# Optimization experiments

Measured on AMD Instinct MI355X. Metric: run time of the kernel, lower is better.

## Reference

```python
import jax, jax.numpy as jnp
import numpy as np

H = 512        # rnn_h
E = 256        # embedding_dim
ATD = 32       # action_type_emb_dim
VOCAB = 50000  # data_agent.wordcnt
NUM_ACTIONS = 10
CHECK_WEIGHT = 1.0
B, SIN, SOUT, Y = 32, 128, 32, 256
DIN = 2 * H + 1 + E + ATD + E  # dec_gru input size (y_in=True, bidir=True)


def gru_step(h, x, Wih, Whh, bih, bhh):
    # PyTorch GRUCell math
    gi = x @ Wih.T + bih
    gh = h @ Whh.T + bhh
    ir, iz, i_n = jnp.split(gi, 3, axis=-1)
    hr, hz, h_n = jnp.split(gh, 3, axis=-1)
    r = jax.nn.sigmoid(ir + hr)
    z = jax.nn.sigmoid(iz + hz)
    n = jnp.tanh(i_n + r * h_n)
    return (1.0 - z) * n + z * h


def setup_inputs() -> dict:
    key = jax.random.key(0)
    ks = iter(jax.random.split(key, 48))

    def p(shape, scale=0.05):
        return jax.random.normal(next(ks), shape, dtype=jnp.float32) * scale

    inp = {}
    inp["x"] = jax.random.randint(next(ks), (B, SIN), 0, VOCAB)
    inp["action_key"] = jax.random.randint(next(ks), (Y,), 0, VOCAB)
    inp["action_type"] = jax.random.randint(next(ks), (Y,), 0, NUM_ACTIONS + 1)
    inp["current_room"] = jax.random.randint(next(ks), (B, SOUT), 0, VOCAB)
    inp["checked"] = jax.random.uniform(next(ks), (B, SOUT + 1, Y), dtype=jnp.float32)
    inp["y"] = jax.random.uniform(next(ks), (B, SOUT, Y), dtype=jnp.float32)
    emb = p((VOCAB, E))
    inp["emb_table"] = emb.at[0].set(0.0)  # padding_idx=0
    inp["atype_table"] = p((NUM_ACTIONS + 1, ATD))
    # encoder GRU, bidirectional, 1 layer
    inp["enc_Wih_f"] = p((3 * H, E)); inp["enc_Whh_f"] = p((3 * H, H))
    inp["enc_bih_f"] = p((3 * H,));   inp["enc_bhh_f"] = p((3 * H,))
    inp["enc_Wih_b"] = p((3 * H, E)); inp["enc_Whh_b"] = p((3 * H, H))
    inp["enc_bih_b"] = p((3 * H,));   inp["enc_bhh_b"] = p((3 * H,))
    inp["trans_W"] = p((E, 2 * H)); inp["trans_b"] = p((E,))
    inp["merge_W"] = p((H, 2 * H)); inp["merge_b"] = p((H,))
    inp["dec_Wih"] = p((3 * H, DIN)); inp["dec_Whh"] = p((3 * H, H))
    inp["dec_bih"] = p((3 * H,));     inp["dec_bhh"] = p((3 * H,))
    inp["dec_W"] = p((1, H)); inp["dec_b"] = p((1,))
    inp["chk_W1"] = p((H, 2 * H + ATD + H)); inp["chk_b1"] = p((H,))
    inp["chk_W2"] = p((1, H));               inp["chk_b2"] = p((1,))
    return inp


def reference(x, action_key, action_type, current_room, checked, y,
              emb_table, atype_table,
              enc_Wih_f, enc_Whh_f, enc_bih_f, enc_bhh_f,
              enc_Wih_b, enc_Whh_b, enc_bih_b, enc_bhh_b,
              trans_W, trans_b, merge_W, merge_b,
              dec_Wih, dec_Whh, dec_bih, dec_bhh, dec_W, dec_b,
              chk_W1, chk_b1, chk_W2, chk_b2):
    emb_out = emb_table[x]  # [B, SIN, E]

    def enc_scan(Wih, Whh, bih, bhh, xs):  # xs: [S, B, E]
        def step(h, xt):
            h2 = gru_step(h, xt, Wih, Whh, bih, bhh)
            return h2, h2
        h0 = jnp.zeros((B, H), emb_out.dtype)
        return jax.lax.scan(step, h0, xs)

    xs = emb_out.transpose(1, 0, 2)
    hT_f, hs_f = enc_scan(enc_Wih_f, enc_Whh_f, enc_bih_f, enc_bhh_f, xs)
    hT_b, hs_b = enc_scan(enc_Wih_b, enc_Whh_b, enc_bih_b, enc_bhh_b, xs[::-1])
    hs_b = hs_b[::-1]
    enc_out = jnp.concatenate([hs_f, hs_b], axis=-1).transpose(1, 0, 2)  # [B, SIN, 2H]

    action_emb = emb_table[action_key]  # [Y, E]
    trans_out = jnp.tanh(enc_out @ trans_W.T + trans_b)  # [B, SIN, E]
    scores = (jnp.einsum('bse,ye->bys', emb_out, action_emb)
              + jnp.einsum('bse,ye->bys', trans_out, action_emb))
    alpha = jax.nn.softmax(scores, axis=-1)
    attention = jnp.einsum('bys,bsd->byd', alpha, enc_out)  # [B, Y, 2H]

    atype_exp = jnp.broadcast_to(atype_table[action_type], (B, Y, ATD))
    room_emb = emb_table[current_room]  # [B, SOUT, E]

    # faithful to torch: hidden [2,B,H].view(B, 2H) (layer-major flatten)
    hidden_cat = jnp.stack([hT_f, hT_b], 0).reshape(B, 2 * H)
    h0_dec = jnp.tanh(hidden_cat @ merge_W.T + merge_b)  # [B, H]
    h_dec = jnp.broadcast_to(h0_dec[:, None, :], (B, Y, H)).reshape(B * Y, H)

    y_prev = jnp.concatenate([jnp.zeros((B, 1, Y), y.dtype), y[:, :-1]], axis=1)

    att_flat = attention.reshape(B * Y, 2 * H)
    at_flat = atype_exp.reshape(B * Y, ATD)

    xs_scan = (checked[:, :SOUT].transpose(1, 0, 2),   # check_in  [T,B,Y]
               room_emb.transpose(1, 0, 2),            # room      [T,B,E]
               y_prev.transpose(1, 0, 2),              # y_{t-1}   [T,B,Y]
               y.transpose(1, 0, 2),                   # y_t       [T,B,Y]
               checked[:, 1:].transpose(1, 0, 2))      # check tgt [T,B,Y]

    def step(h, inputs):
        chk_t, room_t, yp_t, y_t, chk_next = inputs
        room_in = jnp.broadcast_to(room_t[:, None, :], (B, Y, E))
        y_in = jnp.broadcast_to((yp_t @ action_emb)[:, None, :], (B, Y, E))
        dec_in = jnp.concatenate(
            [attention, chk_t[..., None], room_in, atype_exp, y_in], axis=-1
        ).reshape(B * Y, DIN)
        h2 = gru_step(h, dec_in, dec_Wih, dec_Whh, dec_bih, dec_bhh)
        logits = (h2 @ dec_W.T + dec_b).reshape(B, Y)
        logp = jax.nn.log_softmax(logits, axis=1)
        l = -(logp * y_t).sum()
        cat = jnp.concatenate([att_flat, at_flat, h2], axis=1)
        chk = jax.nn.sigmoid(jnp.tanh(cat @ chk_W1.T + chk_b1) @ chk_W2.T + chk_b2).reshape(B, Y)
        cl = -((chk_next * jnp.log(chk) + (1.0 - chk_next) * jnp.log(1.0 - chk)) * y_t).sum() * CHECK_WEIGHT
        return h2, (l, cl)

    _, (ls, cls) = jax.lax.scan(step, h_dec, xs_scan)
    ysum = y.sum()
    loss = ls.sum() / ysum
    check_loss = cls.sum() / ysum
    return (loss + check_loss, loss, check_loss)
```

## Files before the change

kernel.cpp:

```cpp
#include <hip/hip_runtime.h>

typedef unsigned short ushort;
typedef unsigned int uint;
typedef __attribute__((ext_vector_type(8))) short short8;
typedef __attribute__((ext_vector_type(4))) float f32x4;
typedef __attribute__((ext_vector_type(4))) uint u32x4;

#define DEVI __device__ __forceinline__

#define B_ 32
#define SIN_ 128
#define SOUT_ 32
#define Y_ 256
#define H_ 512
#define E_ 256
#define TH_ 1536

DEVI float b2f(ushort u){ return __uint_as_float(((uint)u)<<16); }
DEVI ushort f2b(float f){ uint x = __float_as_uint(f); return (ushort)((x + 0x7FFFu + ((x>>16)&1u)) >> 16); }
DEVI float sigf(float x){ return 1.f/(1.f+__expf(-x)); }
DEVI float tanh_fast(float x){ return 2.f/(1.f+__expf(-2.f*x)) - 1.f; }
DEVI float splus(float x){ return fmaxf(x,0.f) + log1pf(__expf(-fabsf(x))); }
DEVI short8 cvt8(u32x4 v){ return __builtin_bit_cast(short8, v); }

DEVI uint ld_flag(const uint* p){
  uint r;
  asm volatile("global_load_dword %0, %1, off sc0 sc1\n\ts_waitcnt vmcnt(0)"
               : "=v"(r) : "v"(p) : "memory");
  return r;
}
DEVI void st_flag(uint* p, uint v){
  asm volatile("global_store_dword %0, %1, off sc0 sc1" :: "v"(p), "v"(v) : "memory");
}
DEVI void st_h16(ushort* p, uint v){
  asm volatile("global_store_short %0, %1, off sc0 sc1" :: "v"(p), "v"(v) : "memory");
}

__global__ void k_init(float* acc){ if (threadIdx.x < 4) acc[threadIdx.x] = 0.f; }

__global__ void k_wsfail(float* out){ out[0]=1.2345e8f; out[1]=2.3456e8f; out[2]=3.4567e8f; }

__global__ void k_init_enc(uint* __restrict__ flags, ushort* __restrict__ hG)
{
  const int id = blockIdx.x*256 + threadIdx.x;
  if (id < 256) flags[id] = 0u;
  if (id < 16384) ((uint4*)hG)[id] = make_uint4(0,0,0,0);
}

__global__ __launch_bounds__(256) void k_ysum(const float* __restrict__ yv, float* __restrict__ acc)
{
  __shared__ float red[256];
  float s = 0.f;
  for (long i = (long)blockIdx.x*256 + threadIdx.x; i < (long)B_*SOUT_*Y_; i += (long)gridDim.x*256) s += yv[i];
  red[threadIdx.x] = s; __syncthreads();
  for (int o=128;o;o>>=1){ if ((int)threadIdx.x<o) red[threadIdx.x] += red[threadIdx.x+o]; __syncthreads(); }
  if (threadIdx.x==0) atomicAdd(acc+2, red[0]);
}

__global__ void k_lookup(const int* __restrict__ x, const int* __restrict__ akey,
                         const int* __restrict__ atype, const int* __restrict__ croom,
                         const float* __restrict__ yv,
                         const float* __restrict__ emb, const float* __restrict__ attab,
                         ushort* __restrict__ embxs, ushort* __restrict__ aemb,
                         ushort* __restrict__ aembT, float* __restrict__ avec,
                         ushort* __restrict__ acat, ushort* __restrict__ yprev)
{
  const long N1 = (long)SIN_*B_*E_;
  const long N2 = (long)Y_*E_;
  const long N3 = (long)Y_*32;
  const long N4 = (long)SOUT_*B_*E_;
  const long N5 = (long)SOUT_*B_*Y_;
  for (long i = (long)blockIdx.x*blockDim.x + threadIdx.x; i < N1+N2+N3+N4+N5; i += (long)gridDim.x*blockDim.x){
    long id = i;
    if (id < N1){
      int e = id & 255; long sb = id >> 8; int bb = (int)(sb & 31); int s = (int)(sb >> 5);
      embxs[id] = f2b(emb[(size_t)x[bb*SIN_ + s]*E_ + e]);
    } else if ((id -= N1) < N2){
      int e = (int)(id & 255), yy = (int)(id >> 8);
      ushort v = f2b(emb[(size_t)akey[yy]*E_ + e]);
      aemb[yy*E_ + e] = v;
      aembT[e*Y_ + yy] = v;
    } else if ((id -= N2) < N3){
      int a = (int)(id & 31), yy = (int)(id >> 5);
      avec[yy*32 + a] = attab[atype[yy]*32 + a];
    } else if ((id -= N3) < N4){
      int e = (int)(id & 255); long tb = id >> 8; int bb = (int)(tb & 31); int t = (int)(tb >> 5);
      acat[(size_t)tb*512 + e] = f2b(emb[(size_t)croom[bb*SOUT_ + t]*E_ + e]);
    } else { id -= N4;
      int yy = (int)(id & 255); long tb = id >> 8; int bb = (int)(tb & 31); int t = (int)(tb >> 5);
      yprev[id] = (t == 0) ? (ushort)0 : f2b(yv[((size_t)bb*SOUT_ + (t-1))*Y_ + yy]);
    }
  }
}

__global__ __launch_bounds__(256)
void k_convall(const float* __restrict__ eWihF, const float* __restrict__ eWihB,
               const float* __restrict__ transW, const float* __restrict__ dWih,
               const float* __restrict__ cW1, const float* __restrict__ dWhh,
               ushort* __restrict__ WihFb, ushort* __restrict__ WihBb,
               ushort* __restrict__ Wtrb, ushort* __restrict__ Wattb,
               ushort* __restrict__ Wcat2b, ushort* __restrict__ W1attb,
               ushort* __restrict__ Wdecb, ushort* __restrict__ Wchk2b)
{
  const long N1 = 393216;
  const long N2 = 393216;
  const long N3 = 262144;
  const long N4 = 1572864;
  const long N5 = 393216;
  const long N6 = 393216;
  const long N7 = 524288;
  const long N8 = 786432;
  const long N9 = 262144;
  const long NT = N1+N2+N3+N4+N5+N6+N7+N8+N9;
  for (long i = (long)blockIdx.x*256 + threadIdx.x; i < NT; i += (long)gridDim.x*256){
    long id = i;
    if (id < N1){ WihFb[id] = f2b(eWihF[id]); }
    else if ((id -= N1) < N2){ WihBb[id] = f2b(eWihB[id]); }
    else if ((id -= N2) < N3){ Wtrb[id] = f2b(transW[id]); }
    else if ((id -= N3) < N4){
      const long r = id>>10, c = id&1023;
      Wattb[id] = f2b(dWih[r*1569 + c]);
    }
    else if ((id -= N4) < N5){
      const long r = id>>8, c = id&255;
      Wcat2b[r*512 + c] = f2b(dWih[r*1569 + 1025 + c]);
    }
    else if ((id -= N5) < N6){
      const long r = id>>8, c = id&255;
      Wcat2b[r*512 + 256 + c] = f2b(dWih[r*1569 + 1313 + c]);
    }
    else if ((id -= N6) < N7){
      const long r = id>>10, c = id&1023;
      W1attb[id] = f2b(cW1[r*1568 + c]);
    }
    else if ((id -= N7) < N8){ Wdecb[id] = f2b(dWhh[id]); }
    else { id -= N8;
      const long r = id>>9, c = id&511;
      Wchk2b[id] = f2b(cW1[r*1568 + 1056 + c]);
    }
  }
}

__global__ void k_prep2(const float* __restrict__ avec, const float* __restrict__ decWih,
                        const float* __restrict__ dbih, const float* __restrict__ cW1,
                        const float* __restrict__ cb1, const float* __restrict__ dbhh,
                        float* __restrict__ addy, float* __restrict__ addcy,
                        float* __restrict__ wchk, float* __restrict__ dbhhrz)
{
  const long NA = (long)Y_*TH_;
  const long NB = (long)Y_*H_;
  for (long i = (long)blockIdx.x*blockDim.x + threadIdx.x; i < NA+NB+TH_+TH_; i += (long)gridDim.x*blockDim.x){
    long id = i;
    if (id < NA){
      int n = (int)(id % TH_), yy = (int)(id / TH_);
      float s = dbih[n];
      const float* wr = decWih + (size_t)n*1569 + 1281;
      const float* av = avec + yy*32;
      #pragma unroll
      for (int a=0;a<32;++a) s += av[a]*wr[a];
      addy[id] = s;
    } else if ((id -= NA) < NB){
      int n = (int)(id & 511), yy = (int)(id >> 9);
      float s = cb1[n];
      const float* wr = cW1 + (size_t)n*1568 + 1024;
      const float* av = avec + yy*32;
      #pragma unroll
      for (int a=0;a<32;++a) s += av[a]*wr[a];
      addcy[id] = s;
    } else if ((id -= NB) < TH_){
      wchk[id] = decWih[(size_t)id*1569 + 1024];
    } else { id -= TH_;
      dbhhrz[id] = (id < 1024) ? dbhh[id] : 0.f;
    }
  }
}

#define GF_BIAS 1
#define GF_TANH 2
#define GF_WF32 4
#define GF_WBF16 8
#define GF_ADDY 32
#define GF_CHK 64
#define GF_ESUM 128

template<int FLAGS>
__global__ __launch_bounds__(256)
void gemm_nt(const ushort* __restrict__ A, const ushort* __restrict__ W,
             const float* __restrict__ bias,
             const float* __restrict__ addy, int lday,
             float* __restrict__ Cf, ushort* __restrict__ Cb, int ldC,
             int K, int ldA, int ldW, int n0,
             long zA, long zW, long zC,
             const ushort* __restrict__ chkbase)
{
  const int z = blockIdx.z;
  A += (long)z*zA; W += (long)z*zW;
  const int bn = n0 + (blockIdx.x<<7);
  const int bm = (blockIdx.y<<7);
  const int tid = threadIdx.x;
  const int w = tid>>6, lane = tid&63;
  const int wm = (w>>1)<<6, wn = (w&1)<<6;
  const int rs = tid>>1;
  const int kh = (tid&1)<<5;
  __shared__ ushort lsA[8192];
  __shared__ ushort lsB[8192];
  f32x4 acc[4][4];
  #pragma unroll
  for (int i=0;i<4;++i)
    #pragma unroll
    for (int jj=0;jj<4;++jj) acc[i][jj] = 0.f;

  const ushort* pa = A + (size_t)(bm+rs)*ldA + kh;
  const ushort* pb = W + (size_t)(bn+rs)*ldW + kh;
  uint4 va[4], vb[4];
  #pragma unroll
  for (int i=0;i<4;++i){ va[i] = *(const uint4*)(pa + i*8); vb[i] = *(const uint4*)(pb + i*8); }
  const int nkt = K>>6;
  for (int kt=0; kt<nkt; ++kt){
    __syncthreads();
    #pragma unroll
    for (int i=0;i<4;++i){
      const int c = ((tid&1)<<2) + i;
      *(uint4*)&lsA[(size_t)((c<<7) + rs)<<3] = va[i];
      *(uint4*)&lsB[(size_t)((c<<7) + rs)<<3] = vb[i];
    }
    __syncthreads();
    if (kt+1 < nkt){
      const ushort* qa = pa + (size_t)(kt+1)*64;
      const ushort* qb = pb + (size_t)(kt+1)*64;
      #pragma unroll
      for (int i=0;i<4;++i){ va[i] = *(const uint4*)(qa + i*8); vb[i] = *(const uint4*)(qb + i*8); }
    }
    #pragma unroll
    for (int ks=0;ks<2;++ks){
      const int ch = (ks<<2) + (lane>>4);
      short8 af[4], bf[4];
      #pragma unroll
      for (int mi=0;mi<4;++mi) af[mi] = *(const short8*)&lsA[(size_t)((ch<<7) + wm + (mi<<4) + (lane&15))<<3];
      #pragma unroll
      for (int ni=0;ni<4;++ni) bf[ni] = *(const short8*)&lsB[(size_t)((ch<<7) + wn + (ni<<4) + (lane&15))<<3];
      #pragma unroll
      for (int mi=0;mi<4;++mi)
        #pragma unroll
        for (int ni=0;ni<4;++ni)
          acc[mi][ni] = __builtin_amdgcn_mfma_f32_16x16x32_bf16(af[mi], bf[ni], acc[mi][ni], 0,0,0);
    }
  }
  if (FLAGS & GF_CHK){
    float rsum[4][4];
    #pragma unroll
    for (int mi=0;mi<4;++mi)
      #pragma unroll
      for (int q=0;q<4;++q) rsum[mi][q] = 0.f;
    #pragma unroll
    for (int mi=0;mi<4;++mi){
      #pragma unroll
      for (int ni=0;ni<4;++ni){
        const int col = bn + wn + (ni<<4) + (lane&15);
        const float w2v = addy[col];
        const int row0 = bm + wm + (mi<<4) + ((lane>>4)<<2);
        #pragma unroll
        for (int q=0;q<4;++q){
          const float u = acc[mi][ni][q] + b2f(chkbase[(size_t)(row0+q)*H_ + col]);
          rsum[mi][q] += tanh_fast(u) * w2v;
        }
      }
    }
    #pragma unroll
    for (int mi=0;mi<4;++mi)
      #pragma unroll
      for (int q=0;q<4;++q){
        float v = rsum[mi][q];
        v += __shfl_xor(v,1); v += __shfl_xor(v,2); v += __shfl_xor(v,4); v += __shfl_xor(v,8);
        if ((lane&15)==0){
          const int row = bm + wm + (mi<<4) + ((lane>>4)<<2) + q;
          atomicAdd(&Cf[row], v);
        }
      }
  } else {
    const long zc = (long)z*zC;
    #pragma unroll
    for (int mi=0;mi<4;++mi){
      #pragma unroll
      for (int ni=0;ni<4;++ni){
        const int col = bn + wn + (ni<<4) + (lane&15);
        const int row0 = bm + wm + (mi<<4) + ((lane>>4)<<2);
        float bv = 0.f;
        if (FLAGS & GF_BIAS) bv = bias[col];
        #pragma unroll
        for (int q=0;q<4;++q){
          const int row = row0 + q;
          float xv = acc[mi][ni][q] + bv;
          if (FLAGS & GF_ADDY) xv += addy[(size_t)(row&255)*lday + col];
          if (FLAGS & GF_TANH) xv = tanh_fast(xv);
          if (FLAGS & GF_ESUM) xv += b2f(chkbase[((size_t)(row&127)*32 + (row>>7))*256 + col]);
          if (FLAGS & GF_WF32)  Cf[zc + (size_t)row*ldC + col] = xv;
          if (FLAGS & GF_WBF16) Cb[zc + (size_t)row*ldC + col] = f2b(xv);
        }
      }
    }
  }
}

__global__ __launch_bounds__(256,1)
void enc_persist(const float* __restrict__ Wf, const float* __restrict__ Wb,
                 const float* __restrict__ bhf, const float* __restrict__ bhb,
                 const ushort* __restrict__ gif, const ushort* __restrict__ gib,
                 ushort* __restrict__ hG, uint* __restrict__ flags,
                 ushort* __restrict__ encout, ushort* __restrict__ encoutT,
                 float* __restrict__ hTf, float* __restrict__ hTb)
{
  const int g = blockIdx.x;
  const int dir = g >> 5;
  const int j0 = (g & 31) << 4;
  const int tid = threadIdx.x;
  const int w = tid >> 6, lane = tid & 63;
  const int mi = w & 1, kh = w >> 1;
  const int l15 = lane & 15, l4 = lane >> 4;
  const int brow0 = mi*16 + l4*4;

  const float* W = dir ? Wb : Wf;
  const float* bh = dir ? bhb : bhf;
  const ushort* gi = dir ? gib : gif;

  __shared__ __align__(16) float cred[2][3][256];
  __shared__ float bhl[48];

  short8 bw[3][8];
  {
    const int kbase = kh*256 + l4*8;
    #pragma unroll
    for (int ni=0; ni<3; ++ni){
      const float* wr = W + (size_t)(ni*512 + j0 + l15)*512 + kbase;
      #pragma unroll
      for (int ks=0; ks<8; ++ks){
        const float4 f0 = *(const float4*)(wr + ks*32);
        const float4 f1 = *(const float4*)(wr + ks*32 + 4);
        short8 v;
        v[0]=(short)f2b(f0.x); v[1]=(short)f2b(f0.y); v[2]=(short)f2b(f0.z); v[3]=(short)f2b(f0.w);
        v[4]=(short)f2b(f1.x); v[5]=(short)f2b(f1.y); v[6]=(short)f2b(f1.z); v[7]=(short)f2b(f1.w);
        bw[ni][ks] = v;
      }
    }
  }
  if (tid < 48) bhl[tid] = bh[(tid>>4)*512 + j0 + (tid&15)];
  __syncthreads();

  float bh0r=0.f, bh1r=0.f, bh2r=0.f;
  if (kh==0){ bh0r = bhl[l15]; bh1r = bhl[16+l15]; bh2r = bhl[32+l15]; }
  float holdr[4] = {0.f,0.f,0.f,0.f};
  uint* myflag = flags + dir*32 + (g&31);

  for (int t=0; t<128; ++t){
    const int tt = dir ? (127 - t) : t;
    float giv0[4], giv1[4], giv2[4];
    if (kh==0){
      const ushort* girow = gi + ((size_t)tt*32 + brow0)*1536 + j0 + l15;
      #pragma unroll
      for (int q=0; q<4; ++q){
        giv0[q] = b2f(girow[q*1536]);
        giv1[q] = b2f(girow[q*1536 + 512]);
        giv2[q] = b2f(girow[q*1536 + 1024]);
      }
    }
    if (t){
      if ((tid>>6)==2 && (tid&63)<32){
        const uint* fp = flags + dir*32 + (tid&31);
        while (ld_flag(fp) < (uint)t) __builtin_amdgcn_s_sleep(2);
      }
      __syncthreads();
    }
    const ushort* hsrc = hG + ((size_t)((t&1)*2 + dir))*32768 + (size_t)(mi*16+l15)*1024 + kh*256 + l4*8;
    u32x4 a0,a1,a2,a3,a4,a5,a6,a7,b0,b1,b2,b3,b4,b5,b6,b7;
    asm volatile(
      "global_load_dwordx4 %0, %16, off sc0 sc1\n\t"
      "global_load_dwordx4 %1, %16, off offset:64 sc0 sc1\n\t"
      "global_load_dwordx4 %2, %16, off offset:128 sc0 sc1\n\t"
      "global_load_dwordx4 %3, %16, off offset:192 sc0 sc1\n\t"
      "global_load_dwordx4 %4, %16, off offset:256 sc0 sc1\n\t"
      "global_load_dwordx4 %5, %16, off offset:320 sc0 sc1\n\t"
      "global_load_dwordx4 %6, %16, off offset:384 sc0 sc1\n\t"
      "global_load_dwordx4 %7, %16, off offset:448 sc0 sc1\n\t"
      "global_load_dwordx4 %8, %16, off offset:1024 sc0 sc1\n\t"
      "global_load_dwordx4 %9, %16, off offset:1088 sc0 sc1\n\t"
      "global_load_dwordx4 %10, %16, off offset:1152 sc0 sc1\n\t"
      "global_load_dwordx4 %11, %16, off offset:1216 sc0 sc1\n\t"
      "global_load_dwordx4 %12, %16, off offset:1280 sc0 sc1\n\t"
      "global_load_dwordx4 %13, %16, off offset:1344 sc0 sc1\n\t"
      "global_load_dwordx4 %14, %16, off offset:1408 sc0 sc1\n\t"
      "global_load_dwordx4 %15, %16, off offset:1472 sc0 sc1\n\t"
      "s_waitcnt vmcnt(0)"
      : "=&v"(a0),"=&v"(a1),"=&v"(a2),"=&v"(a3),"=&v"(a4),"=&v"(a5),"=&v"(a6),"=&v"(a7),
        "=&v"(b0),"=&v"(b1),"=&v"(b2),"=&v"(b3),"=&v"(b4),"=&v"(b5),"=&v"(b6),"=&v"(b7)
      : "v"(hsrc)
      : "memory");
    const short8 ah[8] = {cvt8(a0),cvt8(a1),cvt8(a2),cvt8(a3),cvt8(a4),cvt8(a5),cvt8(a6),cvt8(a7)};
    const short8 al[8] = {cvt8(b0),cvt8(b1),cvt8(b2),cvt8(b3),cvt8(b4),cvt8(b5),cvt8(b6),cvt8(b7)};
    f32x4 acc[3]; acc[0]=0.f; acc[1]=0.f; acc[2]=0.f;
    #pragma unroll
    for (int ks=0; ks<8; ++ks){
      acc[0] = __builtin_amdgcn_mfma_f32_16x16x32_bf16(ah[ks], bw[0][ks], acc[0],0,0,0);
      acc[1] = __builtin_amdgcn_mfma_f32_16x16x32_bf16(ah[ks], bw[1][ks], acc[1],0,0,0);
      acc[2] = __builtin_amdgcn_mfma_f32_16x16x32_bf16(ah[ks], bw[2][ks], acc[2],0,0,0);
      acc[0] = __builtin_amdgcn_mfma_f32_16x16x32_bf16(al[ks], bw[0][ks], acc[0],0,0,0);
      acc[1] = __builtin_amdgcn_mfma_f32_16x16x32_bf16(al[ks], bw[1][ks], acc[1],0,0,0);
      acc[2] = __builtin_amdgcn_mfma_f32_16x16x32_bf16(al[ks], bw[2][ks], acc[2],0,0,0);
    }
    if (kh==1){
      #pragma unroll
      for (int ni=0; ni<3; ++ni) *(f32x4*)&cred[mi][ni][lane*4] = acc[ni];
    }
    __syncthreads();
    if (kh==0){
      #pragma unroll
      for (int ni=0; ni<3; ++ni){
        const f32x4 o = *(const f32x4*)&cred[mi][ni][lane*4];
        acc[ni][0]+=o[0]; acc[ni][1]+=o[1]; acc[ni][2]+=o[2]; acc[ni][3]+=o[3];
      }
      ushort* dst = hG + ((size_t)(((t+1)&1)*2 + dir))*32768;
      #pragma unroll
      for (int q=0; q<4; ++q){
        const int b = brow0 + q;
        const float r  = sigf(giv0[q] + acc[0][q] + bh0r);
        const float zg = sigf(giv1[q] + acc[1][q] + bh1r);
        const float n  = tanh_fast(giv2[q] + r*(acc[2][q] + bh2r));
        const float h2 = (1.f - zg)*n + zg*holdr[q];
        holdr[q] = h2;
        const ushort hb = f2b(h2);
        const ushort hl = f2b(h2 - b2f(hb));
        if (t < 127){
          st_h16(dst + (size_t)b*1024 + j0 + l15, (uint)hb);
          st_h16(dst + (size_t)b*1024 + 512 + j0 + l15, (uint)hl);
        }
        encout[((size_t)b*SIN_ + tt)*1024 + dir*H_ + j0 + l15] = hb;
        encoutT[((size_t)b*1024 + dir*H_ + j0 + l15)*SIN_ + tt] = hb;
      }
    }
    __syncthreads();
    if (t < 127 && tid == 0) st_flag(myflag, (uint)(t+1));
  }
  if (kh==0){
    float* hT = dir ? hTb : hTf;
    #pragma unroll
    for (int q=0; q<4; ++q) hT[(size_t)(brow0+q)*H_ + j0 + l15] = holdr[q];
  }
}

__global__ __launch_bounds__(256) void k_softmax(const float* __restrict__ sc, ushort* __restrict__ al)
{
  const int row = blockIdx.x*4 + (threadIdx.x>>6);
  const int lane = threadIdx.x&63;
  const float* s = sc + (size_t)row*SIN_;
  const float2 v = *(const float2*)&s[lane*2];
  float m = fmaxf(v.x, v.y);
  #pragma unroll
  for (int o=1;o<64;o<<=1) m = fmaxf(m, __shfl_xor(m, o));
  const float e0 = __expf(v.x - m), e1 = __expf(v.y - m);
  float sum = e0 + e1;
  #pragma unroll
  for (int o=1;o<64;o<<=1) sum += __shfl_xor(sum, o);
  const float inv = 1.f/sum;
  ushort* a = al + (size_t)row*SIN_;
  const uint pkv = (uint)f2b(e0*inv) | ((uint)f2b(e1*inv)<<16);
  *(uint*)&a[lane*2] = pkv;
}

__global__ __launch_bounds__(512)
void k_merge(const float* __restrict__ hTf, const float* __restrict__ hTb,
             const float* __restrict__ mW, const float* __restrict__ mb,
             float* __restrict__ h0)
{
  const int b = blockIdx.x, j = threadIdx.x;
  __shared__ float hc[1024];
  for (int i=j; i<1024; i+=512){
    const int half = i >> 9, jj = i & 511;
    hc[i] = (b < 16) ? hTf[(size_t)(2*b + half)*H_ + jj] : hTb[(size_t)(2*(b-16) + half)*H_ + jj];
  }
  __syncthreads();
  float d = mb[j];
  const float* wr = mW + (size_t)j*1024;
  #pragma unroll 8
  for (int k=0;k<1024;k+=4){
    const float4 a = *(const float4*)&wr[k];
    const float4 hh = *(const float4*)&hc[k];
    d += a.x*hh.x + a.y*hh.y + a.z*hh.z + a.w*hh.w;
  }
  h0[(size_t)b*H_ + j] = tanh_fast(d);
}

__global__ void k_bcast(const float* __restrict__ h0, ushort* __restrict__ hb,
                        float* __restrict__ chkdot, float* __restrict__ logits)
{
  for (long i = (long)blockIdx.x*blockDim.x + threadIdx.x; i < (long)8192*H_; i += (long)gridDim.x*blockDim.x){
    const int jj = (int)(i & 511); const long row = i >> 9; const int bb = (int)(row >> 8);
    hb[i] = f2b(h0[(size_t)bb*H_ + jj]);
    if (i < 8192){ chkdot[i] = 0.f; logits[i] = 0.f; }
  }
}

__global__ __launch_bounds__(512,1)
void gemm_dec(const ushort* __restrict__ A, const ushort* __restrict__ Wd,
              const ushort* __restrict__ gib, const float* __restrict__ sproj_t,
              const float* __restrict__ wchk, const float* __restrict__ dbhh,
              const float* __restrict__ checked, int t,
              const float* __restrict__ decW,
              ushort* __restrict__ h2bo, float* __restrict__ logits)
{
  const int bx = blockIdx.x;
  const int by = blockIdx.y;
  const int bm = by<<7;
  const int tid = threadIdx.x;
  const int w = tid>>6, lane = tid&63;
  const int wrh = w>>2, wc = w&3;
  const int wm = wrh<<6;
  const int l15 = lane&15, l4 = lane>>4;
  __shared__ ushort lsA[128*72];
  __shared__ ushort lsB[384*72];
  f32x4 acc[3][4][2];
  #pragma unroll
  for (int gg=0;gg<3;++gg)
    #pragma unroll
    for (int mi2=0;mi2<4;++mi2)
      #pragma unroll
      for (int ni2=0;ni2<2;++ni2) acc[gg][mi2][ni2] = 0.f;

  const int saRow0 = tid>>3, saK = (tid&7)<<3;
  uint4 va[2], vb[6];
  {
    #pragma unroll
    for (int i=0;i<2;++i){
      const int row = saRow0 + (i<<6);
      va[i] = *(const uint4*)&A[(size_t)(bm+row)*512 + saK];
    }
    #pragma unroll
    for (int i=0;i<6;++i){
      const int s = tid + (i<<9);
      const int gg = s>>10, w1 = s&1023, row = w1>>3, kc = (w1&7)<<3;
      vb[i] = *(const uint4*)&Wd[(size_t)((gg<<9) + (bx<<7) + row)*512 + kc];
    }
  }
  for (int kt=0; kt<8; ++kt){
    __syncthreads();
    #pragma unroll
    for (int i=0;i<2;++i){
      const int row = saRow0 + (i<<6);
      *(uint4*)&lsA[row*72 + saK] = va[i];
    }
    #pragma unroll
    for (int i=0;i<6;++i){
      const int s = tid + (i<<9);
      const int gg = s>>10, w1 = s&1023, row = w1>>3, kc = (w1&7)<<3;
      *(uint4*)&lsB[((gg<<7)+row)*72 + kc] = vb[i];
    }
    __syncthreads();
    if (kt < 7){
      const int ko = (kt+1)<<6;
      #pragma unroll
      for (int i=0;i<2;++i){
        const int row = saRow0 + (i<<6);
        va[i] = *(const uint4*)&A[(size_t)(bm+row)*512 + ko + saK];
      }
      #pragma unroll
      for (int i=0;i<6;++i){
        const int s = tid + (i<<9);
        const int gg = s>>10, w1 = s&1023, row = w1>>3, kc = (w1&7)<<3;
        vb[i] = *(const uint4*)&Wd[(size_t)((gg<<9) + (bx<<7) + row)*512 + ko + kc];
      }
    }
    #pragma unroll
    for (int ks=0;ks<2;++ks){
      short8 af[4];
      #pragma unroll
      for (int mi2=0;mi2<4;++mi2)
        af[mi2] = *(const short8*)&lsA[(wm + (mi2<<4) + l15)*72 + (ks<<5) + (l4<<3)];
      short8 bf[3][2];
      #pragma unroll
      for (int gg=0;gg<3;++gg)
        #pragma unroll
        for (int ni2=0;ni2<2;++ni2)
          bf[gg][ni2] = *(const short8*)&lsB[((gg<<7) + (wc<<5) + (ni2<<4) + l15)*72 + (ks<<5) + (l4<<3)];
      #pragma unroll
      for (int gg=0;gg<3;++gg)
        #pragma unroll
        for (int mi2=0;mi2<4;++mi2)
          #pragma unroll
          for (int ni2=0;ni2<2;++ni2)
            acc[gg][mi2][ni2] = __builtin_amdgcn_mfma_f32_16x16x32_bf16(af[mi2], bf[gg][ni2], acc[gg][mi2][ni2], 0,0,0);
    }
  }
  const int bb = by>>1;
  const float* sp = sproj_t + (size_t)bb*TH_;
  const int jbase = (bx<<7) + (wc<<5);
  float spv[3][2], wcv[3][2], bhnv[2], dwv[2];
  #pragma unroll
  for (int ni2=0;ni2<2;++ni2){
    const int j = jbase + (ni2<<4) + l15;
    spv[0][ni2] = sp[j]; spv[1][ni2] = sp[512+j]; spv[2][ni2] = sp[1024+j];
    wcv[0][ni2] = wchk[j]; wcv[1][ni2] = wchk[512+j]; wcv[2][ni2] = wchk[1024+j];
    bhnv[ni2] = dbhh[1024+j];
    dwv[ni2] = decW[j];
  }
  const float* ckrow = checked + ((size_t)(bb*33 + t))*Y_;
  float lrow[4][4];
  #pragma unroll
  for (int mi2=0;mi2<4;++mi2)
    #pragma unroll
    for (int q=0;q<4;++q) lrow[mi2][q] = 0.f;
  #pragma unroll
  for (int mi2=0;mi2<4;++mi2){
    #pragma unroll
    for (int q=0;q<4;++q){
      const int row = bm + wm + (mi2<<4) + (l4<<2) + q;
      const float ck = ckrow[row & 255];
      #pragma unroll
      for (int ni2=0;ni2<2;++ni2){
        const int j = jbase + (ni2<<4) + l15;
        const float g0 = b2f(gib[(size_t)row*TH_ + j]);
        const float g1 = b2f(gib[(size_t)row*TH_ + 512 + j]);
        const float g2 = b2f(gib[(size_t)row*TH_ + 1024 + j]);
        const float hold = b2f(A[(size_t)row*H_ + j]);
        const float r  = sigf(g0 + spv[0][ni2] + ck*wcv[0][ni2] + acc[0][mi2][ni2][q]);
        const float zg = sigf(g1 + spv[1][ni2] + ck*wcv[1][ni2] + acc[1][mi2][ni2][q]);
        const float n  = tanh_fast(g2 + spv[2][ni2] + ck*wcv[2][ni2] + r*(acc[2][mi2][ni2][q] + bhnv[ni2]));
        const float h2 = (1.f - zg)*n + zg*hold;
        h2bo[(size_t)row*H_ + j] = f2b(h2);
        lrow[mi2][q] += h2 * dwv[ni2];
      }
    }
  }
  #pragma unroll
  for (int mi2=0;mi2<4;++mi2)
    #pragma unroll
    for (int q=0;q<4;++q){
      float v = lrow[mi2][q];
      v += __shfl_xor(v,1); v += __shfl_xor(v,2); v += __shfl_xor(v,4); v += __shfl_xor(v,8);
      if (l15==0){
        const int row = bm + wm + (mi2<<4) + (l4<<2) + q;
        atomicAdd(&logits[row], v);
      }
    }
}

__global__ __launch_bounds__(256)
void dec_loss(float* __restrict__ chkdot, const float* __restrict__ cb2v,
              const float* __restrict__ checked, const float* __restrict__ yv,
              float* __restrict__ logits, int t, float* __restrict__ acc)
{
  const int tid = threadIdx.x;
  if (blockIdx.x < 32){
    const int row = blockIdx.x*256 + tid;
    const int bb = row>>8, yy = row&255;
    const float u = chkdot[row] + cb2v[0];
    chkdot[row] = 0.f;
    const float c = checked[((size_t)bb*33 + (t+1))*Y_ + yy];
    const float yt = yv[((size_t)bb*SOUT_ + t)*Y_ + yy];
    float wv = yt * (c*splus(-u) + (1.f-c)*splus(u));
    __shared__ float red[256];
    red[tid] = wv; __syncthreads();
    for (int o=128;o;o>>=1){ if (tid<o) red[tid] += red[tid+o]; __syncthreads(); }
    if (tid==0) atomicAdd(acc+1, red[0]);
  } else {
    __shared__ float red[256];
    __shared__ float bmx[32], bsm[32];
    const int bb = tid>>3, part = tid&7;
    float lv[32];
    const float* lg = logits + bb*Y_ + part*32;
    float m = -1e30f;
    #pragma unroll
    for (int i=0;i<32;++i){ lv[i] = lg[i]; m = fmaxf(m, lv[i]); }
    red[tid] = m; __syncthreads();
    if (part==0){ float mm = red[tid];
      #pragma unroll
      for (int k2=1;k2<8;++k2) mm = fmaxf(mm, red[tid+k2]);
      bmx[bb] = mm; }
    __syncthreads();
    const float bm = bmx[bb];
    float se = 0.f;
    #pragma unroll
    for (int i=0;i<32;++i) se += __expf(lv[i]-bm);
    red[tid] = se; __syncthreads();
    if (part==0){ float ss = 0.f;
      #pragma unroll
      for (int k2=0;k2<8;++k2) ss += red[tid+k2];
      bsm[bb] = ss; }
    __syncthreads();
    const float lse = bm + logf(bsm[bb]);
    const float* yr = yv + ((size_t)bb*SOUT_ + t)*Y_ + part*32;
    float pl = 0.f;
    #pragma unroll
    for (int i=0;i<32;++i) pl += yr[i]*(lv[i]-lse);
    red[tid] = pl; __syncthreads();
    if (tid==0){ float s = 0.f;
      for (int k2=0;k2<256;++k2) s += red[k2];
      atomicAdd(acc+0, -s); }
    __syncthreads();
    for (int i=tid; i<8192; i+=256) logits[i] = 0.f;
  }
}

__global__ void k_final(const float* __restrict__ acc, float* __restrict__ out)
{
  if (threadIdx.x==0){
    const float ls = acc[0], cls = acc[1], ys = acc[2];
    out[0] = (ls+cls)/ys; out[1] = ls/ys; out[2] = cls/ys;
  }
}

extern "C" void kernel_launch(void* const* d_in, const int* in_sizes, int n_in,
                              void* d_out, int out_size, void* d_ws, size_t ws_size,
                              hipStream_t stream)
{
  (void)in_sizes; (void)n_in; (void)out_size;
  const int*   x      = (const int*)d_in[0];
  const int*   akey   = (const int*)d_in[1];
  const int*   atype  = (const int*)d_in[2];
  const int*   croom  = (const int*)d_in[3];
  const float* checked= (const float*)d_in[4];
  const float* yv     = (const float*)d_in[5];
  const float* emb    = (const float*)d_in[6];
  const float* attab  = (const float*)d_in[7];
  const float* eWihF  = (const float*)d_in[8];
  const float* eWhhF  = (const float*)d_in[9];
  const float* ebihF  = (const float*)d_in[10];
  const float* ebhhF  = (const float*)d_in[11];
  const float* eWihB  = (const float*)d_in[12];
  const float* eWhhB  = (const float*)d_in[13];
  const float* ebihB  = (const float*)d_in[14];
  const float* ebhhB  = (const float*)d_in[15];
  const float* transW = (const float*)d_in[16];
  const float* transb = (const float*)d_in[17];
  const float* mergeW = (const float*)d_in[18];
  const float* mergeb = (const float*)d_in[19];
  const float* dWih   = (const float*)d_in[20];
  const float* dWhh   = (const float*)d_in[21];
  const float* dbih   = (const float*)d_in[22];
  const float* dbhh   = (const float*)d_in[23];
  const float* dW     = (const float*)d_in[24];
  const float* cW1    = (const float*)d_in[26];
  const float* cb1    = (const float*)d_in[27];
  const float* cW2    = (const float*)d_in[28];
  const float* cb2    = (const float*)d_in[29];

  char* base = (char*)d_ws;
  size_t off = 0;
  auto alloc = [&](size_t bytes)->char*{ char* p = base + off; off += (bytes + 255) & ~(size_t)255; return p; };

  float*  accv   = (float*)alloc(256);
  ushort* embxs  = (ushort*)alloc((size_t)SIN_*B_*E_*2);
  ushort* aemb   = (ushort*)alloc((size_t)Y_*E_*2);
  ushort* aembT  = (ushort*)alloc((size_t)Y_*E_*2);
  float*  avec   = (float*)alloc((size_t)Y_*32*4);
  ushort* yprev  = (ushort*)alloc((size_t)SOUT_*B_*Y_*2);
  ushort* acat   = (ushort*)alloc((size_t)SOUT_*B_*512*2);
  ushort* gi_fb  = (ushort*)alloc((size_t)2*SIN_*B_*TH_*2);
  ushort* gi_f   = gi_fb;
  ushort* gi_b   = gi_fb + (size_t)SIN_*B_*TH_;
  ushort* gibase = gi_fb;
  ushort* encout = (ushort*)alloc((size_t)B_*SIN_*1024*2);
  ushort* encoutT= (ushort*)alloc((size_t)B_*1024*SIN_*2);
  float*  hTf    = (float*)alloc((size_t)B_*H_*4);
  float*  hTb    = (float*)alloc((size_t)B_*H_*4);
  float*  h0dec  = (float*)alloc((size_t)B_*H_*4);
  ushort* esum   = (ushort*)alloc((size_t)B_*SIN_*E_*2);
  float*  scores = (float*)alloc((size_t)B_*Y_*SIN_*4);
  ushort* alpha  = (ushort*)alloc((size_t)B_*Y_*SIN_*2);
  ushort* att    = (ushort*)alloc((size_t)8192*1024*2);
  ushort* chkbase= (ushort*)alloc((size_t)8192*H_*2);
  float*  addy   = (float*)alloc((size_t)Y_*TH_*4);
  float*  addcy  = (float*)alloc((size_t)Y_*H_*4);
  float*  sproj  = (float*)alloc((size_t)SOUT_*B_*TH_*4);
  float*  wchk   = (float*)alloc((size_t)TH_*4);
  float*  dbhhrz = (float*)alloc((size_t)TH_*4);
  ushort* WihFb  = (ushort*)alloc((size_t)TH_*E_*2);
  ushort* WihBb  = (ushort*)alloc((size_t)TH_*E_*2);
  ushort* Wtrb   = (ushort*)alloc((size_t)E_*1024*2);
  ushort* Wattb  = (ushort*)alloc((size_t)TH_*1024*2);
  ushort* Wcat2b = (ushort*)alloc((size_t)TH_*512*2);
  ushort* W1attb = (ushort*)alloc((size_t)H_*1024*2);
  ushort* Wdecb  = (ushort*)alloc((size_t)TH_*512*2);
  ushort* Wchk2b = (ushort*)alloc((size_t)512*512*2);
  ushort* h2bA   = (ushort*)alloc((size_t)8192*H_*2);
  ushort* h2bB   = (ushort*)alloc((size_t)8192*H_*2);
  float*  chkdot = (float*)alloc((size_t)8192*4);
  float*  logits = (float*)alloc((size_t)8192*4);
  ushort* hG     = (ushort*)alloc((size_t)2*2*32*1024*2);
  uint*   flags  = (uint*)alloc((size_t)256*4);

  if (off > ws_size){ k_wsfail<<<1,1,0,stream>>>((float*)d_out); return; }

  float* outp = (float*)d_out;

  k_init<<<dim3(1), dim3(64), 0, stream>>>(accv);
  k_init_enc<<<dim3(64), dim3(256), 0, stream>>>(flags, hG);
  k_ysum<<<dim3(256), dim3(256), 0, stream>>>(yv, accv);
  k_lookup<<<dim3(2048), dim3(256), 0, stream>>>(x, akey, atype, croom, yv, emb, attab,
                                                 embxs, aemb, aembT, avec, acat, yprev);
  k_convall<<<dim3(2048), dim3(256), 0, stream>>>(eWihF, eWihB, transW, dWih, cW1, dWhh,
                                                  WihFb, WihBb, Wtrb, Wattb, Wcat2b, W1attb, Wdecb, Wchk2b);
  k_prep2<<<dim3(1024), dim3(256), 0, stream>>>(avec, dWih, dbih, cW1, cb1, dbhh,
                                                addy, addcy, wchk, dbhhrz);

  gemm_nt<(GF_BIAS|GF_WBF16)><<<dim3(12,32,1), dim3(256), 0, stream>>>(
    embxs, WihFb, ebihF, nullptr, 0, nullptr, gi_f, TH_, E_, E_, E_, 0, 0L,0L,0L, nullptr);
  gemm_nt<(GF_BIAS|GF_WBF16)><<<dim3(12,32,1), dim3(256), 0, stream>>>(
    embxs, WihBb, ebihB, nullptr, 0, nullptr, gi_b, TH_, E_, E_, E_, 0, 0L,0L,0L, nullptr);

  enc_persist<<<dim3(64), dim3(256), 0, stream>>>(eWhhF, eWhhB, ebhhF, ebhhB, gi_f, gi_b,
                                                  hG, flags, encout, encoutT, hTf, hTb);

  gemm_nt<(GF_BIAS|GF_TANH|GF_ESUM|GF_WBF16)><<<dim3(2,32,1), dim3(256), 0, stream>>>(
    encout, Wtrb, transb, nullptr, 0, nullptr, esum, E_, 1024, 1024, 1024, 0, 0L,0L,0L, embxs);

  gemm_nt<GF_WF32><<<dim3(1,2,32), dim3(256), 0, stream>>>(
    aemb, esum, nullptr, nullptr, 0, scores, nullptr, SIN_, E_, E_, E_, 0,
    0L, (long)SIN_*E_, (long)Y_*SIN_, nullptr);
  k_softmax<<<dim3(2048), dim3(256), 0, stream>>>(scores, alpha);

  gemm_nt<GF_WBF16><<<dim3(8,2,32), dim3(256), 0, stream>>>(
    alpha, encoutT, nullptr, nullptr, 0, nullptr, att, 1024, SIN_, SIN_, SIN_, 0,
    (long)Y_*SIN_, (long)1024*SIN_, (long)Y_*1024, nullptr);

  k_merge<<<dim3(32), dim3(512), 0, stream>>>(hTf, hTb, mergeW, mergeb, h0dec);

  gemm_nt<GF_WBF16><<<dim3(2,8,1), dim3(256), 0, stream>>>(
    yprev, aembT, nullptr, nullptr, 0, nullptr, acat+256, 512, Y_, Y_, Y_, 0, 0L,0L,0L, nullptr);
  gemm_nt<(GF_BIAS|GF_WF32)><<<dim3(12,8,1), dim3(256), 0, stream>>>(
    acat, Wcat2b, dbhhrz, nullptr, 0, sproj, nullptr, TH_, 512, 512, 512, 0, 0L,0L,0L, nullptr);

  gemm_nt<(GF_WBF16|GF_ADDY)><<<dim3(12,64,1), dim3(256), 0, stream>>>(
    att, Wattb, nullptr, addy, TH_, nullptr, gibase, TH_, 1024, 1024, 1024, 0, 0L,0L,0L, nullptr);
  gemm_nt<(GF_WBF16|GF_ADDY)><<<dim3(4,64,1), dim3(256), 0, stream>>>(
    att, W1attb, nullptr, addcy, H_, nullptr, chkbase, H_, 1024, 1024, 1024, 0, 0L,0L,0L, nullptr);

  k_bcast<<<dim3(4096), dim3(256), 0, stream>>>(h0dec, h2bA, chkdot, logits);

  for (int t=0; t<SOUT_; ++t){
    ushort* hin_b  = (t&1) ? h2bB : h2bA;
    ushort* hout_b = (t&1) ? h2bA : h2bB;
    gemm_dec<<<dim3(4,64), dim3(512), 0, stream>>>(
      hin_b, Wdecb, gibase, sproj + (size_t)t*B_*TH_, wchk, dbhh, checked, t,
      dW, hout_b, logits);
    gemm_nt<GF_CHK><<<dim3(4,64), dim3(256), 0, stream>>>(
      hout_b, Wchk2b, nullptr, cW2, 0, chkdot, nullptr, 0, 512, 512, 512, 0,
      0L,0L,0L, chkbase);
    dec_loss<<<dim3(33), dim3(256), 0, stream>>>(chkdot, cb2, checked, yv, logits, t, accv);
  }
  k_final<<<dim3(1), dim3(1), 0, stream>>>(accv, outp);
}
```

Before: 4.077 ms.

## Drop encoder hi/lo hidden split and fuse decoder step kernels with skewed check pipeline

The encoder recurrence stops carrying a bf16 low-order correction term, which halves the per-step hidden-state loads and MFMA count, and it moves the encout stores after the flag signal. The decoder loop merges the GRU GEMM, the check-head GEMM and the loss reduction into one 320-block launch per step. Blocks 256 and up compute the check head for the previous step while the other 256 blocks run the current GRU step, and a last-block counter does the loss reduction using double-buffered logits. This removes two launches per step and overlaps the check head with the recurrence, at the cost of lower precision in the encoder hidden state and more complex cross-block synchronisation.

```diff
diff --git a/kernel.cpp b/kernel.cpp
--- a/kernel.cpp
+++ b/kernel.cpp
@@ -35,6 +35,19 @@
 DEVI void st_h16(ushort* p, uint v){
   asm volatile("global_store_short %0, %1, off sc0 sc1" :: "v"(p), "v"(v) : "memory");
 }
+DEVI void stf_sc1(float* p, float v){
+  asm volatile("global_store_dword %0, %1, off sc0 sc1" :: "v"(p), "v"(__float_as_uint(v)) : "memory");
+}
+DEVI void ld16_sc1(const float* p, float* o){
+  u32x4 r0,r1,r2,r3;
+  asm volatile("global_load_dwordx4 %0, %4, off sc0 sc1\n\t"
+               "global_load_dwordx4 %1, %4, off offset:16 sc0 sc1\n\t"
+               "global_load_dwordx4 %2, %4, off offset:32 sc0 sc1\n\t"
+               "global_load_dwordx4 %3, %4, off offset:48 sc0 sc1\n\t"
+               "s_waitcnt vmcnt(0)"
+               : "=&v"(r0),"=&v"(r1),"=&v"(r2),"=&v"(r3) : "v"(p) : "memory");
+  *(u32x4*)(o) = r0; *(u32x4*)(o+4) = r1; *(u32x4*)(o+8) = r2; *(u32x4*)(o+12) = r3;
+}
 
 __global__ void k_init(float* acc){ if (threadIdx.x < 4) acc[threadIdx.x] = 0.f; }
 
@@ -44,7 +57,7 @@
 {
   const int id = blockIdx.x*256 + threadIdx.x;
   if (id < 256) flags[id] = 0u;
-  if (id < 16384) ((uint4*)hG)[id] = make_uint4(0,0,0,0);
+  if (id < 8192) ((uint4*)hG)[id] = make_uint4(0,0,0,0);
 }
 
 __global__ __launch_bounds__(256) void k_ysum(const float* __restrict__ yv, float* __restrict__ acc)
@@ -180,7 +193,6 @@
 #define GF_WF32 4
 #define GF_WBF16 8
 #define GF_ADDY 32
-#define GF_CHK 64
 #define GF_ESUM 128
 
 template<int FLAGS>
@@ -246,57 +258,24 @@
           acc[mi][ni] = __builtin_amdgcn_mfma_f32_16x16x32_bf16(af[mi], bf[ni], acc[mi][ni], 0,0,0);
     }
   }
-  if (FLAGS & GF_CHK){
-    float rsum[4][4];
-    #pragma unroll
-    for (int mi=0;mi<4;++mi)
-      #pragma unroll
-      for (int q=0;q<4;++q) rsum[mi][q] = 0.f;
-    #pragma unroll
-    for (int mi=0;mi<4;++mi){
-      #pragma unroll
-      for (int ni=0;ni<4;++ni){
-        const int col = bn + wn + (ni<<4) + (lane&15);
-        const float w2v = addy[col];
-        const int row0 = bm + wm + (mi<<4) + ((lane>>4)<<2);
-        #pragma unroll
-        for (int q=0;q<4;++q){
-          const float u = acc[mi][ni][q] + b2f(chkbase[(size_t)(row0+q)*H_ + col]);
-          rsum[mi][q] += tanh_fast(u) * w2v;
-        }
-      }
-    }
-    #pragma unroll
-    for (int mi=0;mi<4;++mi)
+  const long zc = (long)z*zC;
+  #pragma unroll
+  for (int mi=0;mi<4;++mi){
+    #pragma unroll
+    for (int ni=0;ni<4;++ni){
+      const int col = bn + wn + (ni<<4) + (lane&15);
+      const int row0 = bm + wm + (mi<<4) + ((lane>>4)<<2);
+      float bv = 0.f;
+      if (FLAGS & GF_BIAS) bv = bias[col];
       #pragma unroll
       for (int q=0;q<4;++q){
-        float v = rsum[mi][q];
-        v += __shfl_xor(v,1); v += __shfl_xor(v,2); v += __shfl_xor(v,4); v += __shfl_xor(v,8);
-        if ((lane&15)==0){
-          const int row = bm + wm + (mi<<4) + ((lane>>4)<<2) + q;
-          atomicAdd(&Cf[row], v);
-        }
-      }
-  } else {
-    const long zc = (long)z*zC;
-    #pragma unroll
-    for (int mi=0;mi<4;++mi){
-      #pragma unroll
-      for (int ni=0;ni<4;++ni){
-        const int col = bn + wn + (ni<<4) + (lane&15);
-        const int row0 = bm + wm + (mi<<4) + ((lane>>4)<<2);
-        float bv = 0.f;
-        if (FLAGS & GF_BIAS) bv = bias[col];
-        #pragma unroll
-        for (int q=0;q<4;++q){
-          const int row = row0 + q;
-          float xv = acc[mi][ni][q] + bv;
-          if (FLAGS & GF_ADDY) xv += addy[(size_t)(row&255)*lday + col];
-          if (FLAGS & GF_TANH) xv = tanh_fast(xv);
-          if (FLAGS & GF_ESUM) xv += b2f(chkbase[((size_t)(row&127)*32 + (row>>7))*256 + col]);
-          if (FLAGS & GF_WF32)  Cf[zc + (size_t)row*ldC + col] = xv;
-          if (FLAGS & GF_WBF16) Cb[zc + (size_t)row*ldC + col] = f2b(xv);
-        }
+        const int row = row0 + q;
+        float xv = acc[mi][ni][q] + bv;
+        if (FLAGS & GF_ADDY) xv += addy[(size_t)(row&255)*lday + col];
+        if (FLAGS & GF_TANH) xv = tanh_fast(xv);
+        if (FLAGS & GF_ESUM) xv += b2f(chkbase[((size_t)(row&127)*32 + (row>>7))*256 + col]);
+        if (FLAGS & GF_WF32)  Cf[zc + (size_t)row*ldC + col] = xv;
+        if (FLAGS & GF_WBF16) Cb[zc + (size_t)row*ldC + col] = f2b(xv);
       }
     }
   }
@@ -370,54 +349,42 @@
       }
       __syncthreads();
     }
-    const ushort* hsrc = hG + ((size_t)((t&1)*2 + dir))*32768 + (size_t)(mi*16+l15)*1024 + kh*256 + l4*8;
-    u32x4 a0,a1,a2,a3,a4,a5,a6,a7,b0,b1,b2,b3,b4,b5,b6,b7;
+    const ushort* hsrc = hG + ((size_t)((t&1)*2 + dir))*16384 + (size_t)(mi*16+l15)*512 + kh*256 + l4*8;
+    u32x4 a0,a1,a2,a3,a4,a5,a6,a7;
     asm volatile(
-      "global_load_dwordx4 %0, %16, off sc0 sc1\n\t"
-      "global_load_dwordx4 %1, %16, off offset:64 sc0 sc1\n\t"
-      "global_load_dwordx4 %2, %16, off offset:128 sc0 sc1\n\t"
-      "global_load_dwordx4 %3, %16, off offset:192 sc0 sc1\n\t"
-      "global_load_dwordx4 %4, %16, off offset:256 sc0 sc1\n\t"
-      "global_load_dwordx4 %5, %16, off offset:320 sc0 sc1\n\t"
-      "global_load_dwordx4 %6, %16, off offset:384 sc0 sc1\n\t"
-      "global_load_dwordx4 %7, %16, off offset:448 sc0 sc1\n\t"
-      "global_load_dwordx4 %8, %16, off offset:1024 sc0 sc1\n\t"
-      "global_load_dwordx4 %9, %16, off offset:1088 sc0 sc1\n\t"
-      "global_load_dwordx4 %10, %16, off offset:1152 sc0 sc1\n\t"
-      "global_load_dwordx4 %11, %16, off offset:1216 sc0 sc1\n\t"
-      "global_load_dwordx4 %12, %16, off offset:1280 sc0 sc1\n\t"
-      "global_load_dwordx4 %13, %16, off offset:1344 sc0 sc1\n\t"
-      "global_load_dwordx4 %14, %16, off offset:1408 sc0 sc1\n\t"
-      "global_load_dwordx4 %15, %16, off offset:1472 sc0 sc1\n\t"
+      "global_load_dwordx4 %0, %8, off sc0 sc1\n\t"
+      "global_load_dwordx4 %1, %8, off offset:64 sc0 sc1\n\t"
+      "global_load_dwordx4 %2, %8, off offset:128 sc0 sc1\n\t"
+      "global_load_dwordx4 %3, %8, off offset:192 sc0 sc1\n\t"
+      "global_load_dwordx4 %4, %8, off offset:256 sc0 sc1\n\t"
+      "global_load_dwordx4 %5, %8, off offset:320 sc0 sc1\n\t"
+      "global_load_dwordx4 %6, %8, off offset:384 sc0 sc1\n\t"
+      "global_load_dwordx4 %7, %8, off offset:448 sc0 sc1\n\t"
       "s_waitcnt vmcnt(0)"
-      : "=&v"(a0),"=&v"(a1),"=&v"(a2),"=&v"(a3),"=&v"(a4),"=&v"(a5),"=&v"(a6),"=&v"(a7),
-        "=&v"(b0),"=&v"(b1),"=&v"(b2),"=&v"(b3),"=&v"(b4),"=&v"(b5),"=&v"(b6),"=&v"(b7)
+      : "=&v"(a0),"=&v"(a1),"=&v"(a2),"=&v"(a3),"=&v"(a4),"=&v"(a5),"=&v"(a6),"=&v"(a7)
       : "v"(hsrc)
       : "memory");
     const short8 ah[8] = {cvt8(a0),cvt8(a1),cvt8(a2),cvt8(a3),cvt8(a4),cvt8(a5),cvt8(a6),cvt8(a7)};
-    const short8 al[8] = {cvt8(b0),cvt8(b1),cvt8(b2),cvt8(b3),cvt8(b4),cvt8(b5),cvt8(b6),cvt8(b7)};
     f32x4 acc[3]; acc[0]=0.f; acc[1]=0.f; acc[2]=0.f;
     #pragma unroll
     for (int ks=0; ks<8; ++ks){
       acc[0] = __builtin_amdgcn_mfma_f32_16x16x32_bf16(ah[ks], bw[0][ks], acc[0],0,0,0);
       acc[1] = __builtin_amdgcn_mfma_f32_16x16x32_bf16(ah[ks], bw[1][ks], acc[1],0,0,0);
       acc[2] = __builtin_amdgcn_mfma_f32_16x16x32_bf16(ah[ks], bw[2][ks], acc[2],0,0,0);
-      acc[0] = __builtin_amdgcn_mfma_f32_16x16x32_bf16(al[ks], bw[0][ks], acc[0],0,0,0);
-      acc[1] = __builtin_amdgcn_mfma_f32_16x16x32_bf16(al[ks], bw[1][ks], acc[1],0,0,0);
-      acc[2] = __builtin_amdgcn_mfma_f32_16x16x32_bf16(al[ks], bw[2][ks], acc[2],0,0,0);
     }
     if (kh==1){
       #pragma unroll
       for (int ni=0; ni<3; ++ni) *(f32x4*)&cred[mi][ni][lane*4] = acc[ni];
     }
     __syncthreads();
+    ushort hbs[4];
     if (kh==0){
       #pragma unroll
       for (int ni=0; ni<3; ++ni){
         const f32x4 o = *(const f32x4*)&cred[mi][ni][lane*4];
         acc[ni][0]+=o[0]; acc[ni][1]+=o[1]; acc[ni][2]+=o[2]; acc[ni][3]+=o[3];
       }
-      ushort* dst = hG + ((size_t)(((t+1)&1)*2 + dir))*32768;
+      ushort* dst = hG + ((size_t)(((t+1)&1)*2 + dir))*16384;
       #pragma unroll
       for (int q=0; q<4; ++q){
         const int b = brow0 + q;
@@ -427,17 +394,20 @@
         const float h2 = (1.f - zg)*n + zg*holdr[q];
         holdr[q] = h2;
         const ushort hb = f2b(h2);
-        const ushort hl = f2b(h2 - b2f(hb));
-        if (t < 127){
-          st_h16(dst + (size_t)b*1024 + j0 + l15, (uint)hb);
-          st_h16(dst + (size_t)b*1024 + 512 + j0 + l15, (uint)hl);
-        }
-        encout[((size_t)b*SIN_ + tt)*1024 + dir*H_ + j0 + l15] = hb;
-        encoutT[((size_t)b*1024 + dir*H_ + j0 + l15)*SIN_ + tt] = hb;
+        hbs[q] = hb;
+        if (t < 127) st_h16(dst + (size_t)b*512 + j0 + l15, (uint)hb);
       }
     }
     __syncthreads();
     if (t < 127 && tid == 0) st_flag(myflag, (uint)(t+1));
+    if (kh==0){
+      #pragma unroll
+      for (int q=0; q<4; ++q){
+        const int b = brow0 + q;
+        encout[((size_t)b*SIN_ + tt)*1024 + dir*H_ + j0 + l15] = hbs[q];
+        encoutT[((size_t)b*1024 + dir*H_ + j0 + l15)*SIN_ + tt] = hbs[q];
+      }
+    }
   }
   if (kh==0){
     float* hT = dir ? hTb : hTf;
@@ -489,212 +459,313 @@
 }
 
 __global__ void k_bcast(const float* __restrict__ h0, ushort* __restrict__ hb,
-                        float* __restrict__ chkdot, float* __restrict__ logits)
+                        float* __restrict__ L0, float* __restrict__ L1, uint* __restrict__ counter)
 {
   for (long i = (long)blockIdx.x*blockDim.x + threadIdx.x; i < (long)8192*H_; i += (long)gridDim.x*blockDim.x){
     const int jj = (int)(i & 511); const long row = i >> 9; const int bb = (int)(row >> 8);
     hb[i] = f2b(h0[(size_t)bb*H_ + jj]);
-    if (i < 8192){ chkdot[i] = 0.f; logits[i] = 0.f; }
+    if (i < 8192){ L0[i] = 0.f; L1[i] = 0.f; }
+    if (i == 0) counter[0] = 0u;
   }
 }
 
 __global__ __launch_bounds__(512,1)
-void gemm_dec(const ushort* __restrict__ A, const ushort* __restrict__ Wd,
-              const ushort* __restrict__ gib, const float* __restrict__ sproj_t,
-              const float* __restrict__ wchk, const float* __restrict__ dbhh,
-              const float* __restrict__ checked, int t,
+void dec_step(const ushort* __restrict__ hin, ushort* __restrict__ hout,
+              const ushort* __restrict__ Wd, const ushort* __restrict__ gib,
+              const float* __restrict__ sproj_t, const float* __restrict__ wchk,
+              const float* __restrict__ dbhh, const float* __restrict__ checked,
               const float* __restrict__ decW,
-              ushort* __restrict__ h2bo, float* __restrict__ logits)
-{
-  const int bx = blockIdx.x;
-  const int by = blockIdx.y;
-  const int bm = by<<7;
+              const ushort* __restrict__ Wchk2b, const ushort* __restrict__ chkbase,
+              const float* __restrict__ cw2, const float* __restrict__ cb2v,
+              const float* __restrict__ yv,
+              float* __restrict__ logitsW, float* __restrict__ logitsR,
+              float* __restrict__ chkdot, uint* __restrict__ counter,
+              float* __restrict__ accv, int tstep)
+{
+  __shared__ __align__(16) ushort smem[36864];
+  __shared__ uint slast;
   const int tid = threadIdx.x;
-  const int w = tid>>6, lane = tid&63;
-  const int wrh = w>>2, wc = w&3;
-  const int wm = wrh<<6;
-  const int l15 = lane&15, l4 = lane>>4;
-  __shared__ ushort lsA[128*72];
-  __shared__ ushort lsB[384*72];
-  f32x4 acc[3][4][2];
-  #pragma unroll
-  for (int gg=0;gg<3;++gg)
-    #pragma unroll
-    for (int mi2=0;mi2<4;++mi2)
-      #pragma unroll
-      for (int ni2=0;ni2<2;++ni2) acc[gg][mi2][ni2] = 0.f;
-
-  const int saRow0 = tid>>3, saK = (tid&7)<<3;
-  uint4 va[2], vb[6];
-  {
-    #pragma unroll
-    for (int i=0;i<2;++i){
-      const int row = saRow0 + (i<<6);
-      va[i] = *(const uint4*)&A[(size_t)(bm+row)*512 + saK];
-    }
-    #pragma unroll
-    for (int i=0;i<6;++i){
-      const int s = tid + (i<<9);
-      const int gg = s>>10, w1 = s&1023, row = w1>>3, kc = (w1&7)<<3;
-      vb[i] = *(const uint4*)&Wd[(size_t)((gg<<9) + (bx<<7) + row)*512 + kc];
-    }
-  }
-  for (int kt=0; kt<8; ++kt){
-    __syncthreads();
-    #pragma unroll
-    for (int i=0;i<2;++i){
-      const int row = saRow0 + (i<<6);
-      *(uint4*)&lsA[row*72 + saK] = va[i];
-    }
-    #pragma unroll
-    for (int i=0;i<6;++i){
-      const int s = tid + (i<<9);
-      const int gg = s>>10, w1 = s&1023, row = w1>>3, kc = (w1&7)<<3;
-      *(uint4*)&lsB[((gg<<7)+row)*72 + kc] = vb[i];
-    }
-    __syncthreads();
-    if (kt < 7){
-      const int ko = (kt+1)<<6;
+
+  if (blockIdx.x < 256){
+    if (tstep >= SOUT_) return;
+    const int bx = blockIdx.x & 3;
+    const int by = blockIdx.x >> 2;
+    const int bm = by<<7;
+    const int w = tid>>6, lane = tid&63;
+    const int wrh = w>>2, wc = w&3;
+    const int wm = wrh<<6;
+    const int l15 = lane&15, l4 = lane>>4;
+    ushort* lsA = smem;
+    ushort* lsB = smem + 128*72;
+    f32x4 acc[3][4][2];
+    #pragma unroll
+    for (int gg=0;gg<3;++gg)
+      #pragma unroll
+      for (int mi2=0;mi2<4;++mi2)
+        #pragma unroll
+        for (int ni2=0;ni2<2;++ni2) acc[gg][mi2][ni2] = 0.f;
+
+    const int saRow0 = tid>>3, saK = (tid&7)<<3;
+    uint4 va[2], vb[6];
+    {
       #pragma unroll
       for (int i=0;i<2;++i){
         const int row = saRow0 + (i<<6);
-        va[i] = *(const uint4*)&A[(size_t)(bm+row)*512 + ko + saK];
+        va[i] = *(const uint4*)&hin[(size_t)(bm+row)*512 + saK];
       }
       #pragma unroll
       for (int i=0;i<6;++i){
         const int s = tid + (i<<9);
         const int gg = s>>10, w1 = s&1023, row = w1>>3, kc = (w1&7)<<3;
-        vb[i] = *(const uint4*)&Wd[(size_t)((gg<<9) + (bx<<7) + row)*512 + ko + kc];
-      }
-    }
-    #pragma unroll
-    for (int ks=0;ks<2;++ks){
-      short8 af[4];
-      #pragma unroll
-      for (int mi2=0;mi2<4;++mi2)
-        af[mi2] = *(const short8*)&lsA[(wm + (mi2<<4) + l15)*72 + (ks<<5) + (l4<<3)];
-      short8 bf[3][2];
-      #pragma unroll
-      for (int gg=0;gg<3;++gg)
-        #pragma unroll
-        for (int ni2=0;ni2<2;++ni2)
-          bf[gg][ni2] = *(const short8*)&lsB[((gg<<7) + (wc<<5) + (ni2<<4) + l15)*72 + (ks<<5) + (l4<<3)];
-      #pragma unroll
-      for (int gg=0;gg<3;++gg)
+        vb[i] = *(const uint4*)&Wd[(size_t)((gg<<9) + (bx<<7) + row)*512 + kc];
+      }
+    }
+    for (int kt=0; kt<8; ++kt){
+      __syncthreads();
+      #pragma unroll
+      for (int i=0;i<2;++i){
+        const int row = saRow0 + (i<<6);
+        *(uint4*)&lsA[row*72 + saK] = va[i];
+      }
+      #pragma unroll
+      for (int i=0;i<6;++i){
+        const int s = tid + (i<<9);
+        const int gg = s>>10, w1 = s&1023, row = w1>>3, kc = (w1&7)<<3;
+        *(uint4*)&lsB[((gg<<7)+row)*72 + kc] = vb[i];
+      }
+      __syncthreads();
+      if (kt < 7){
+        const int ko = (kt+1)<<6;
+        #pragma unroll
+        for (int i=0;i<2;++i){
+          const int row = saRow0 + (i<<6);
+          va[i] = *(const uint4*)&hin[(size_t)(bm+row)*512 + ko + saK];
+        }
+        #pragma unroll
+        for (int i=0;i<6;++i){
+          const int s = tid + (i<<9);
+          const int gg = s>>10, w1 = s&1023, row = w1>>3, kc = (w1&7)<<3;
+          vb[i] = *(const uint4*)&Wd[(size_t)((gg<<9) + (bx<<7) + row)*512 + ko + kc];
+        }
+      }
+      #pragma unroll
+      for (int ks=0;ks<2;++ks){
+        short8 af[4];
         #pragma unroll
         for (int mi2=0;mi2<4;++mi2)
+          af[mi2] = *(const short8*)&lsA[(wm + (mi2<<4) + l15)*72 + (ks<<5) + (l4<<3)];
+        short8 bf[3][2];
+        #pragma unroll
+        for (int gg=0;gg<3;++gg)
           #pragma unroll
           for (int ni2=0;ni2<2;++ni2)
-            acc[gg][mi2][ni2] = __builtin_amdgcn_mfma_f32_16x16x32_bf16(af[mi2], bf[gg][ni2], acc[gg][mi2][ni2], 0,0,0);
-    }
-  }
-  const int bb = by>>1;
-  const float* sp = sproj_t + (size_t)bb*TH_;
-  const int jbase = (bx<<7) + (wc<<5);
-  float spv[3][2], wcv[3][2], bhnv[2], dwv[2];
-  #pragma unroll
-  for (int ni2=0;ni2<2;++ni2){
-    const int j = jbase + (ni2<<4) + l15;
-    spv[0][ni2] = sp[j]; spv[1][ni2] = sp[512+j]; spv[2][ni2] = sp[1024+j];
-    wcv[0][ni2] = wchk[j]; wcv[1][ni2] = wchk[512+j]; wcv[2][ni2] = wchk[1024+j];
-    bhnv[ni2] = dbhh[1024+j];
-    dwv[ni2] = decW[j];
-  }
-  const float* ckrow = checked + ((size_t)(bb*33 + t))*Y_;
-  float lrow[4][4];
-  #pragma unroll
-  for (int mi2=0;mi2<4;++mi2)
-    #pragma unroll
-    for (int q=0;q<4;++q) lrow[mi2][q] = 0.f;
-  #pragma unroll
-  for (int mi2=0;mi2<4;++mi2){
-    #pragma unroll
-    for (int q=0;q<4;++q){
-      const int row = bm + wm + (mi2<<4) + (l4<<2) + q;
-      const float ck = ckrow[row & 255];
-      #pragma unroll
-      for (int ni2=0;ni2<2;++ni2){
-        const int j = jbase + (ni2<<4) + l15;
-        const float g0 = b2f(gib[(size_t)row*TH_ + j]);
-        const float g1 = b2f(gib[(size_t)row*TH_ + 512 + j]);
-        const float g2 = b2f(gib[(size_t)row*TH_ + 1024 + j]);
-        const float hold = b2f(A[(size_t)row*H_ + j]);
-        const float r  = sigf(g0 + spv[0][ni2] + ck*wcv[0][ni2] + acc[0][mi2][ni2][q]);
-        const float zg = sigf(g1 + spv[1][ni2] + ck*wcv[1][ni2] + acc[1][mi2][ni2][q]);
-        const float n  = tanh_fast(g2 + spv[2][ni2] + ck*wcv[2][ni2] + r*(acc[2][mi2][ni2][q] + bhnv[ni2]));
-        const float h2 = (1.f - zg)*n + zg*hold;
-        h2bo[(size_t)row*H_ + j] = f2b(h2);
-        lrow[mi2][q] += h2 * dwv[ni2];
-      }
-    }
-  }
-  #pragma unroll
-  for (int mi2=0;mi2<4;++mi2)
-    #pragma unroll
-    for (int q=0;q<4;++q){
-      float v = lrow[mi2][q];
-      v += __shfl_xor(v,1); v += __shfl_xor(v,2); v += __shfl_xor(v,4); v += __shfl_xor(v,8);
-      if (l15==0){
+            bf[gg][ni2] = *(const short8*)&lsB[((gg<<7) + (wc<<5) + (ni2<<4) + l15)*72 + (ks<<5) + (l4<<3)];
+        #pragma unroll
+        for (int gg=0;gg<3;++gg)
+          #pragma unroll
+          for (int mi2=0;mi2<4;++mi2)
+            #pragma unroll
+            for (int ni2=0;ni2<2;++ni2)
+              acc[gg][mi2][ni2] = __builtin_amdgcn_mfma_f32_16x16x32_bf16(af[mi2], bf[gg][ni2], acc[gg][mi2][ni2], 0,0,0);
+      }
+    }
+    const int bb = by>>1;
+    const float* sp = sproj_t + (size_t)bb*TH_;
+    const int jbase = (bx<<7) + (wc<<5);
+    float spv[3][2], wcv[3][2], bhnv[2], dwv[2];
+    #pragma unroll
+    for (int ni2=0;ni2<2;++ni2){
+      const int j = jbase + (ni2<<4) + l15;
+      spv[0][ni2] = sp[j]; spv[1][ni2] = sp[512+j]; spv[2][ni2] = sp[1024+j];
+      wcv[0][ni2] = wchk[j]; wcv[1][ni2] = wchk[512+j]; wcv[2][ni2] = wchk[1024+j];
+      bhnv[ni2] = dbhh[1024+j];
+      dwv[ni2] = decW[j];
+    }
+    const float* ckrow = checked + ((size_t)(bb*33 + tstep))*Y_;
+    float lrow[4][4];
+    #pragma unroll
+    for (int mi2=0;mi2<4;++mi2)
+      #pragma unroll
+      for (int q=0;q<4;++q) lrow[mi2][q] = 0.f;
+    #pragma unroll
+    for (int mi2=0;mi2<4;++mi2){
+      #pragma unroll
+      for (int q=0;q<4;++q){
         const int row = bm + wm + (mi2<<4) + (l4<<2) + q;
-        atomicAdd(&logits[row], v);
-      }
-    }
-}
-
-__global__ __launch_bounds__(256)
-void dec_loss(float* __restrict__ chkdot, const float* __restrict__ cb2v,
-              const float* __restrict__ checked, const float* __restrict__ yv,
-              float* __restrict__ logits, int t, float* __restrict__ acc)
-{
-  const int tid = threadIdx.x;
-  if (blockIdx.x < 32){
-    const int row = blockIdx.x*256 + tid;
-    const int bb = row>>8, yy = row&255;
-    const float u = chkdot[row] + cb2v[0];
-    chkdot[row] = 0.f;
-    const float c = checked[((size_t)bb*33 + (t+1))*Y_ + yy];
-    const float yt = yv[((size_t)bb*SOUT_ + t)*Y_ + yy];
-    float wv = yt * (c*splus(-u) + (1.f-c)*splus(u));
-    __shared__ float red[256];
-    red[tid] = wv; __syncthreads();
-    for (int o=128;o;o>>=1){ if (tid<o) red[tid] += red[tid+o]; __syncthreads(); }
-    if (tid==0) atomicAdd(acc+1, red[0]);
+        const float ck = ckrow[row & 255];
+        #pragma unroll
+        for (int ni2=0;ni2<2;++ni2){
+          const int j = jbase + (ni2<<4) + l15;
+          const float g0 = b2f(gib[(size_t)row*TH_ + j]);
+          const float g1 = b2f(gib[(size_t)row*TH_ + 512 + j]);
+          const float g2 = b2f(gib[(size_t)row*TH_ + 1024 + j]);
+          const float hold = b2f(hin[(size_t)row*H_ + j]);
+          const float r  = sigf(g0 + spv[0][ni2] + ck*wcv[0][ni2] + acc[0][mi2][ni2][q]);
+          const float zg = sigf(g1 + spv[1][ni2] + ck*wcv[1][ni2] + acc[1][mi2][ni2][q]);
+          const float n  = tanh_fast(g2 + spv[2][ni2] + ck*wcv[2][ni2] + r*(acc[2][mi2][ni2][q] + bhnv[ni2]));
+          const float h2 = (1.f - zg)*n + zg*hold;
+          hout[(size_t)row*H_ + j] = f2b(h2);
+          lrow[mi2][q] += h2 * dwv[ni2];
+        }
+      }
+    }
+    #pragma unroll
+    for (int mi2=0;mi2<4;++mi2)
+      #pragma unroll
+      for (int q=0;q<4;++q){
+        float v = lrow[mi2][q];
+        v += __shfl_xor(v,1); v += __shfl_xor(v,2); v += __shfl_xor(v,4); v += __shfl_xor(v,8);
+        if (l15==0){
+          const int row = bm + wm + (mi2<<4) + (l4<<2) + q;
+          atomicAdd(&logitsW[row], v);
+        }
+      }
   } else {
-    __shared__ float red[256];
-    __shared__ float bmx[32], bsm[32];
-    const int bb = tid>>3, part = tid&7;
-    float lv[32];
-    const float* lg = logits + bb*Y_ + part*32;
-    float m = -1e30f;
-    #pragma unroll
-    for (int i=0;i<32;++i){ lv[i] = lg[i]; m = fmaxf(m, lv[i]); }
-    red[tid] = m; __syncthreads();
-    if (part==0){ float mm = red[tid];
-      #pragma unroll
-      for (int k2=1;k2<8;++k2) mm = fmaxf(mm, red[tid+k2]);
-      bmx[bb] = mm; }
+    if (tstep == 0) return;
+    const int km1 = tstep - 1;
+    const int cid = blockIdx.x - 256;
+    const int bm = cid<<7;
+    const int half = tid>>8;
+    const int tidh = tid&255;
+    const int w4 = tidh>>6, lane = tidh&63;
+    const int wm = (w4>>1)<<6, wn = (w4&1)<<6;
+    const int rs = tidh>>1;
+    const int khh = (tidh&1)<<5;
+    const int l15 = lane&15, l4 = lane>>4;
+    ushort* lsA = smem + half*16384;
+    ushort* lsB = lsA + 8192;
+    float rsum[4][4];
+    #pragma unroll
+    for (int mi=0;mi<4;++mi)
+      #pragma unroll
+      for (int q=0;q<4;++q) rsum[mi][q] = 0.f;
+
+    for (int p=0;p<2;++p){
+      const int bn = ((p<<1) + half)<<7;
+      f32x4 acc[4][4];
+      #pragma unroll
+      for (int i=0;i<4;++i)
+        #pragma unroll
+        for (int jj=0;jj<4;++jj) acc[i][jj] = 0.f;
+      const ushort* pa = hin + (size_t)(bm+rs)*512 + khh;
+      const ushort* pb = Wchk2b + (size_t)(bn+rs)*512 + khh;
+      uint4 va[4], vb[4];
+      #pragma unroll
+      for (int i=0;i<4;++i){ va[i] = *(const uint4*)(pa + i*8); vb[i] = *(const uint4*)(pb + i*8); }
+      for (int kt=0; kt<8; ++kt){
+        __syncthreads();
+        #pragma unroll
+        for (int i=0;i<4;++i){
+          const int c = ((tidh&1)<<2) + i;
+          *(uint4*)&lsA[(size_t)((c<<7) + rs)<<3] = va[i];
+          *(uint4*)&lsB[(size_t)((c<<7) + rs)<<3] = vb[i];
+        }
+        __syncthreads();
+        if (kt < 7){
+          const ushort* qa = pa + (size_t)(kt+1)*64;
+          const ushort* qb = pb + (size_t)(kt+1)*64;
+          #pragma unroll
+          for (int i=0;i<4;++i){ va[i] = *(const uint4*)(qa + i*8); vb[i] = *(const uint4*)(qb + i*8); }
+        }
+        #pragma unroll
+        for (int ks=0;ks<2;++ks){
+          const int ch = (ks<<2) + l4;
+          short8 af[4], bf[4];
+          #pragma unroll
+          for (int mi=0;mi<4;++mi) af[mi] = *(const short8*)&lsA[(size_t)((ch<<7) + wm + (mi<<4) + l15)<<3];
+          #pragma unroll
+          for (int ni=0;ni<4;++ni) bf[ni] = *(const short8*)&lsB[(size_t)((ch<<7) + wn + (ni<<4) + l15)<<3];
+          #pragma unroll
+          for (int mi=0;mi<4;++mi)
+            #pragma unroll
+            for (int ni=0;ni<4;++ni)
+              acc[mi][ni] = __builtin_amdgcn_mfma_f32_16x16x32_bf16(af[mi], bf[ni], acc[mi][ni], 0,0,0);
+        }
+      }
+      #pragma unroll
+      for (int mi=0;mi<4;++mi){
+        #pragma unroll
+        for (int ni=0;ni<4;++ni){
+          const int col = bn + wn + (ni<<4) + l15;
+          const float w2v = cw2[col];
+          const int row0 = bm + wm + (mi<<4) + (l4<<2);
+          #pragma unroll
+          for (int q=0;q<4;++q){
+            const float u = acc[mi][ni][q] + b2f(chkbase[(size_t)(row0+q)*H_ + col]);
+            rsum[mi][q] += tanh_fast(u) * w2v;
+          }
+        }
+      }
+    }
     __syncthreads();
-    const float bm = bmx[bb];
-    float se = 0.f;
-    #pragma unroll
-    for (int i=0;i<32;++i) se += __expf(lv[i]-bm);
-    red[tid] = se; __syncthreads();
-    if (part==0){ float ss = 0.f;
-      #pragma unroll
-      for (int k2=0;k2<8;++k2) ss += red[tid+k2];
-      bsm[bb] = ss; }
+    float* cred2 = (float*)smem;
+    #pragma unroll
+    for (int mi=0;mi<4;++mi)
+      #pragma unroll
+      for (int q=0;q<4;++q){
+        float v = rsum[mi][q];
+        v += __shfl_xor(v,1); v += __shfl_xor(v,2); v += __shfl_xor(v,4); v += __shfl_xor(v,8);
+        if (l15==0){
+          const int widx = half*2 + (wn>>6);
+          cred2[widx*128 + wm + (mi<<4) + (l4<<2) + q] = v;
+        }
+      }
     __syncthreads();
-    const float lse = bm + logf(bsm[bb]);
-    const float* yr = yv + ((size_t)bb*SOUT_ + t)*Y_ + part*32;
-    float pl = 0.f;
-    #pragma unroll
-    for (int i=0;i<32;++i) pl += yr[i]*(lv[i]-lse);
-    red[tid] = pl; __syncthreads();
-    if (tid==0){ float s = 0.f;
-      for (int k2=0;k2<256;++k2) s += red[k2];
-      atomicAdd(acc+0, -s); }
+    if (tid < 128){
+      const float tot = cred2[tid] + cred2[128+tid] + cred2[256+tid] + cred2[384+tid];
+      stf_sc1(chkdot + bm + tid, tot);
+    }
     __syncthreads();
-    for (int i=tid; i<8192; i+=256) logits[i] = 0.f;
+    if (tid==0) slast = atomicAdd(counter, 1u);
+    __syncthreads();
+    if (slast != 63u) return;
+
+    float* sm = (float*)smem;
+    float wsum = 0.f;
+    {
+      const int r0 = tid*16;
+      float cd[16];
+      ld16_sc1(chkdot + r0, cd);
+      const float b2v = cb2v[0];
+      #pragma unroll
+      for (int i=0;i<16;++i){
+        const int row = r0 + i, bb = row>>8, yy = row&255;
+        const float u = cd[i] + b2v;
+        const float c = checked[((size_t)bb*33 + km1 + 1)*Y_ + yy];
+        const float yt = yv[((size_t)bb*SOUT_ + km1)*Y_ + yy];
+        wsum += yt * (c*splus(-u) + (1.f-c)*splus(u));
+      }
+    }
+    sm[tid] = wsum; __syncthreads();
+    for (int o=256;o;o>>=1){ if (tid<o) sm[tid] += sm[tid+o]; __syncthreads(); }
+    if (tid==0) atomicAdd(accv+1, sm[0]);
+    __syncthreads();
+    {
+      const int bb = tid>>4, part = tid&15;
+      const float* lg = logitsR + bb*Y_ + part*16;
+      float lv[16];
+      float m = -1e30f;
+      #pragma unroll
+      for (int i=0;i<16;++i){ lv[i] = lg[i]; m = fmaxf(m, lv[i]); }
+      m = fmaxf(m, __shfl_xor(m,1)); m = fmaxf(m, __shfl_xor(m,2));
+      m = fmaxf(m, __shfl_xor(m,4)); m = fmaxf(m, __shfl_xor(m,8));
+      float se = 0.f;
+      #pragma unroll
+      for (int i=0;i<16;++i) se += __expf(lv[i]-m);
+      se += __shfl_xor(se,1); se += __shfl_xor(se,2); se += __shfl_xor(se,4); se += __shfl_xor(se,8);
+      const float lse = m + logf(se);
+      const float* yr = yv + ((size_t)bb*SOUT_ + km1)*Y_ + part*16;
+      float pl = 0.f;
+      #pragma unroll
+      for (int i=0;i<16;++i) pl += yr[i]*(lv[i]-lse);
+      pl += __shfl_xor(pl,1); pl += __shfl_xor(pl,2); pl += __shfl_xor(pl,4); pl += __shfl_xor(pl,8);
+      sm[tid] = (part==0) ? pl : 0.f;
+    }
+    __syncthreads();
+    for (int o=256;o;o>>=1){ if (tid<o) sm[tid] += sm[tid+o]; __syncthreads(); }
+    if (tid==0) atomicAdd(accv+0, -sm[0]);
+    for (int i=tid; i<8192; i+=512) logitsR[i] = 0.f;
+    if (tid==0) counter[0] = 0u;
   }
 }
 
@@ -782,9 +853,11 @@
   ushort* h2bA   = (ushort*)alloc((size_t)8192*H_*2);
   ushort* h2bB   = (ushort*)alloc((size_t)8192*H_*2);
   float*  chkdot = (float*)alloc((size_t)8192*4);
-  float*  logits = (float*)alloc((size_t)8192*4);
-  ushort* hG     = (ushort*)alloc((size_t)2*2*32*1024*2);
+  float*  L0     = (float*)alloc((size_t)8192*4);
+  float*  L1     = (float*)alloc((size_t)8192*4);
+  ushort* hG     = (ushort*)alloc((size_t)2*2*32*512*2);
   uint*   flags  = (uint*)alloc((size_t)256*4);
+  uint*   counter= (uint*)alloc((size_t)256);
 
   if (off > ws_size){ k_wsfail<<<1,1,0,stream>>>((float*)d_out); return; }
 
@@ -832,18 +905,17 @@
   gemm_nt<(GF_WBF16|GF_ADDY)><<<dim3(4,64,1), dim3(256), 0, stream>>>(
     att, W1attb, nullptr, addcy, H_, nullptr, chkbase, H_, 1024, 1024, 1024, 0, 0L,0L,0L, nullptr);
 
-  k_bcast<<<dim3(4096), dim3(256), 0, stream>>>(h0dec, h2bA, chkdot, logits);
-
-  for (int t=0; t<SOUT_; ++t){
-    ushort* hin_b  = (t&1) ? h2bB : h2bA;
-    ushort* hout_b = (t&1) ? h2bA : h2bB;
-    gemm_dec<<<dim3(4,64), dim3(512), 0, stream>>>(
-      hin_b, Wdecb, gibase, sproj + (size_t)t*B_*TH_, wchk, dbhh, checked, t,
-      dW, hout_b, logits);
-    gemm_nt<GF_CHK><<<dim3(4,64), dim3(256), 0, stream>>>(
-      hout_b, Wchk2b, nullptr, cW2, 0, chkdot, nullptr, 0, 512, 512, 512, 0,
-      0L,0L,0L, chkbase);
-    dec_loss<<<dim3(33), dim3(256), 0, stream>>>(chkdot, cb2, checked, yv, logits, t, accv);
+  k_bcast<<<dim3(4096), dim3(256), 0, stream>>>(h0dec, h2bA, L0, L1, counter);
+
+  for (int k=0; k<=SOUT_; ++k){
+    const ushort* hin = (k&1) ? h2bB : h2bA;
+    ushort* hout      = (k&1) ? h2bA : h2bB;
+    float* LW = (k&1) ? L1 : L0;
+    float* LR = (k&1) ? L0 : L1;
+    const int ks = (k < SOUT_) ? k : (SOUT_-1);
+    dec_step<<<dim3(320), dim3(512), 0, stream>>>(
+      hin, hout, Wdecb, gibase, sproj + (size_t)ks*B_*TH_, wchk, dbhh, checked,
+      dW, Wchk2b, chkbase, cW2, cb2, yv, LW, LR, chkdot, counter, accv, k);
   }
   k_final<<<dim3(1), dim3(1), 0, stream>>>(accv, outp);
 }
```

New measurement: 6.659 ms. 1.63x slower.
